# Kernel optimization log

Measured on AMD Instinct MI355X. Metric: run time of the kernel, lower is better.

Reference implementation:

```python
import jax, jax.numpy as jnp
import numpy as np

B, IN, O, F, FH = 512, 2000, 64, 8, 32
D = 64 + FH * O  # 2112


def setup_inputs() -> dict:
    key = jax.random.key(0)
    ks = jax.random.split(key, 17)
    rn = lambda k, s: jax.random.normal(k, s, dtype=jnp.float32) * 0.05
    return dict(
        x=rn(ks[0], (B, IN)),
        fc_in_W=rn(ks[1], (1024, IN)), fc_in_b=rn(ks[2], (1024,)),
        fc1_W=rn(ks[3], (128, 1024)), fc1_b=rn(ks[4], (128,)),
        out1_W=rn(ks[5], (O, 64, 128)), out1_b=rn(ks[6], (O, 64)),
        coef_nn_W=rn(ks[7], (F, FH, 1)), coef_nn_b=rn(ks[8], (F, FH)),
        coef_att_W=rn(ks[9], (F, FH, FH)),
        out_att_W=rn(ks[10], (O, FH, FH)),
        nodes_trans_W=rn(ks[11], (O, O)),
        trans_gcn_W=rn(ks[12], (D, D)),
        outmap_W=rn(ks[13], (1, D)), outmap_b=rn(ks[14], (1,)),
        prelu_a=jnp.float32(0.25),
        coef_m=rn(ks[15], (O, O, F)),
    )


def reference(x, fc_in_W, fc_in_b, fc1_W, fc1_b, out1_W, out1_b,
              coef_nn_W, coef_nn_b, coef_att_W, out_att_W,
              nodes_trans_W, trans_gcn_W, outmap_W, outmap_b, prelu_a, coef_m):
    elu = jax.nn.elu
    # trunk MLP
    h = jax.nn.relu(x @ fc_in_W.T + fc_in_b)          # [B,1024]
    h = jax.nn.relu(h @ fc1_W.T + fc1_b)              # [B,128]
    # per-output-node heads (vectorized over the output_dim loop)
    hiddens = jax.nn.relu(jnp.einsum('bk,odk->bod', h, out1_W) + out1_b)  # [B,O,64]
    # per-feature coef embedding: Linear(1,FH) on each coef_m[:,:,i] slice
    cf = elu(coef_m[..., None] * coef_nn_W[:, :, 0] + coef_nn_b)          # [O,O,F,FH]
    # sum over concatenated feature axis (F*FH) of exp(elu(.))
    s = jnp.exp(elu(cf)).sum(axis=(2, 3))[:, :, None, None]               # [O,O,1,1]
    lin = jnp.einsum('xyfh,fgh->xyfg', cf, coef_att_W)                    # per-feature attention linear
    p = elu(jnp.exp(elu(cf)) * lin / s)
    cfs = elu(p.sum(axis=2) / F)                                          # [O,O,FH]
    # node-level attention (vectorized over the output_dim loop)
    coef_sum = jnp.exp(elu(cfs)).sum(axis=1)                              # [O,FH]
    p2 = jnp.exp(elu(cfs)) / coef_sum[:, None, :]                         # [O,O,FH]
    lin2 = jnp.einsum('oih,igh->oig', cfs, out_att_W)
    att = (p2 * lin2).reshape(O, O * FH)                                  # concat over i (i-major)
    hc = jnp.concatenate(
        [hiddens, jnp.broadcast_to(att[None], (x.shape[0], O, O * FH))], axis=2)  # [B,O,D]
    nt = jnp.einsum('bpd,op->bod', hc, nodes_trans_W)                     # node mixing Linear(O,O)
    trans = jax.nn.sigmoid(jnp.einsum('bod,ed->boe', nt, trans_gcn_W))    # [B,O,D]
    z = (trans @ outmap_W.T + outmap_b).squeeze(-1)                       # [B,O]
    return jnp.where(z >= 0, z, prelu_a * z)                              # PReLU
```

## Files before the change

### kernel.cpp

```cpp
#include <hip/hip_runtime.h>
#include <math.h>

typedef __attribute__((ext_vector_type(8))) short bf16x8;
typedef __attribute__((ext_vector_type(4))) float f32x4;

static __device__ __forceinline__ float fast_elu(float x) {
    return x > 0.0f ? x : __expf(x) - 1.0f;
}

static __device__ __forceinline__ unsigned short f2bf(float f) {
    unsigned int u = __float_as_uint(f);
    unsigned int r = (u + 0x7FFFu + ((u >> 16) & 1u)) >> 16;
    return (unsigned short)r;
}

static __device__ __forceinline__ bf16x8 cvt8(const float* __restrict__ s) {
    float4 a = *reinterpret_cast<const float4*>(s);
    float4 b = *reinterpret_cast<const float4*>(s + 4);
    bf16x8 r;
    r[0] = (short)f2bf(a.x); r[1] = (short)f2bf(a.y);
    r[2] = (short)f2bf(a.z); r[3] = (short)f2bf(a.w);
    r[4] = (short)f2bf(b.x); r[5] = (short)f2bf(b.y);
    r[6] = (short)f2bf(b.z); r[7] = (short)f2bf(b.w);
    return r;
}

#define S0 131072
#define S1 393216
#define S2 409600
#define S3 410112
#define S4 475648
#define S5 492544
#define CONV_BLOCKS 1924

static __device__ __forceinline__ void conv_phase(
    int bx,
    const float* __restrict__ x, const float* __restrict__ fcinW,
    const float* __restrict__ fc1W, const float* __restrict__ ntW,
    const float* __restrict__ out1W, const float* __restrict__ tgw,
    unsigned short* __restrict__ xb, unsigned short* __restrict__ fcinWb,
    unsigned short* __restrict__ fc1Wb, unsigned short* __restrict__ Wb,
    unsigned short* __restrict__ out1WbT, unsigned short* __restrict__ Gb)
{
    int u = bx * 256 + threadIdx.x;
    if (u < S0) {
        int r = u >> 8, c = u & 255;
        bf16x8 v;
        if (c < 250) v = cvt8(&x[(size_t)r * 2000 + c * 8]);
        else { bf16x8 z = {0,0,0,0,0,0,0,0}; v = z; }
        *reinterpret_cast<bf16x8*>(&xb[(size_t)r * 2048 + c * 8]) = v;
    } else if (u < S1) {
        int i = u - S0;
        int r = i >> 8, c = i & 255;
        bf16x8 v;
        if (c < 250) v = cvt8(&fcinW[(size_t)r * 2000 + c * 8]);
        else { bf16x8 z = {0,0,0,0,0,0,0,0}; v = z; }
        *reinterpret_cast<bf16x8*>(&fcinWb[(size_t)r * 2048 + c * 8]) = v;
    } else if (u < S2) {
        int i8 = (u - S1) * 8;
        *reinterpret_cast<bf16x8*>(&fc1Wb[i8]) = cvt8(&fc1W[i8]);
    } else if (u < S3) {
        int i8 = (u - S2) * 8;
        *reinterpret_cast<bf16x8*>(&Wb[i8]) = cvt8(&ntW[i8]);
    } else if (u < S4) {
        int i = u - S3;
        int n = i >> 4, kc = i & 15;
        int d = n >> 6, p = n & 63;
        *reinterpret_cast<bf16x8*>(&out1WbT[(size_t)n * 128 + kc * 8]) =
            cvt8(&out1W[(size_t)((p << 6) | d) * 128 + kc * 8]);
    } else if (u < S5) {
        int i = u - S4;
        int e = i >> 3, c = i & 7;
        *reinterpret_cast<bf16x8*>(&Gb[(size_t)e * 64 + c * 8]) =
            cvt8(&tgw[(size_t)e * 2112 + c * 8]);
    }
}

static __device__ __forceinline__ void coef_phase(
    int bx, float* __restrict__ smemf,
    const float* __restrict__ coef_m, const float* __restrict__ cW,
    const float* __restrict__ cB, const float* __restrict__ attW,
    float* __restrict__ cfs)
{
    float* cf_s = smemf;
    float* part = smemf + 1024;
    const int t = threadIdx.x;
    const int wv = t >> 6, lane = t & 63;
    const int xy = bx * 4 + wv;
    float ls = 0.0f;
    #pragma unroll
    for (int i = 0; i < 4; ++i) {
        int idx = i * 64 + lane;
        int f = idx >> 5;
        float v = fast_elu(coef_m[xy * 8 + f] * cW[idx] + cB[idx]);
        cf_s[wv * 256 + idx] = v;
        ls += __expf(fast_elu(v));
    }
    #pragma unroll
    for (int m = 1; m < 64; m <<= 1) ls += __shfl_xor(ls, m, 64);
    __syncthreads();
    const float rs = __builtin_amdgcn_rcpf(ls);
    const int g = lane & 31, fg = lane >> 5;
    float acc = 0.0f;
    for (int f = fg * 4; f < fg * 4 + 4; ++f) {
        float lin = 0.0f;
        #pragma unroll
        for (int h = 0; h < 32; h += 4) {
            float4 Lv = *reinterpret_cast<const float4*>(&cf_s[wv * 256 + f * 32 + h]);
            float4 Wv = *reinterpret_cast<const float4*>(&attW[f * 1024 + g * 32 + h]);
            lin += Lv.x * Wv.x + Lv.y * Wv.y + Lv.z * Wv.z + Lv.w * Wv.w;
        }
        float e = __expf(fast_elu(cf_s[wv * 256 + f * 32 + g]));
        acc += fast_elu(e * lin * rs);
    }
    part[wv * 64 + lane] = acc;
    __syncthreads();
    if (lane < 32) {
        float tot = part[wv * 64 + lane] + part[wv * 64 + lane + 32];
        cfs[xy * 32 + lane] = fast_elu(tot * 0.125f);
    }
}

static __device__ __forceinline__ void att_phase(
    int o, int ic, float* __restrict__ smemf,
    const float* __restrict__ cfs, const float* __restrict__ oattW,
    float* __restrict__ att)
{
    float* L    = smemf;
    float* red  = smemf + 2048;
    float* csum = smemf + 2304;
    const int t = threadIdx.x;
    #pragma unroll
    for (int j = 0; j < 8; ++j) L[t + 256 * j] = cfs[o * 2048 + t + 256 * j];
    __syncthreads();
    {
        int h = t & 31, ig = t >> 5;
        float ps = 0.0f;
        for (int i = ig * 8; i < ig * 8 + 8; ++i) ps += __expf(fast_elu(L[i * 32 + h]));
        red[t] = ps;
        __syncthreads();
        if (t < 32) {
            float cs = 0.0f;
            #pragma unroll
            for (int j = 0; j < 8; ++j) cs += red[j * 32 + t];
            csum[t] = cs;
        }
        __syncthreads();
    }
    int idx = ic * 256 + t;
    int i = idx >> 5, g = idx & 31;
    float lin2 = 0.0f;
    #pragma unroll
    for (int h = 0; h < 32; h += 4) {
        float4 Lv = *reinterpret_cast<const float4*>(&L[i * 32 + h]);
        float4 Wv = *reinterpret_cast<const float4*>(&oattW[i * 1024 + g * 32 + h]);
        lin2 += Lv.x * Wv.x + Lv.y * Wv.y + Lv.z * Wv.z + Lv.w * Wv.w;
    }
    float p2 = __expf(fast_elu(L[idx])) * __builtin_amdgcn_rcpf(csum[g]);
    att[o * 2048 + idx] = p2 * lin2;
}

static __device__ __forceinline__ void natt_phase(
    int bx, float* __restrict__ smemf,
    const float* __restrict__ ntW, const float* __restrict__ att,
    unsigned short* __restrict__ nattb)
{
    float* ntW_s = smemf;
    float* att_s = smemf + 64 * 65;
    const int t = threadIdx.x;
    const int d0 = bx * 16;
    #pragma unroll
    for (int j = 0; j < 16; ++j) {
        int idx = t + 256 * j;
        ntW_s[(idx >> 6) * 65 + (idx & 63)] = ntW[idx];
    }
    #pragma unroll
    for (int j = 0; j < 4; ++j) {
        int idx = t + 256 * j;
        int p = idx >> 4, dd = idx & 15;
        att_s[p * 17 + dd] = att[p * 2048 + d0 + dd];
    }
    __syncthreads();
    const int dd = t & 15, ob = (t >> 4) * 4;
    float acc[4] = {0.0f, 0.0f, 0.0f, 0.0f};
    for (int p = 0; p < 64; ++p) {
        float av = att_s[p * 17 + dd];
        #pragma unroll
        for (int i = 0; i < 4; ++i) acc[i] += ntW_s[(ob + i) * 65 + p] * av;
    }
    #pragma unroll
    for (int i = 0; i < 4; ++i)
        nattb[(ob + i) * 2048 + d0 + dd] = f2bf(acc[i]);
}

static __device__ __forceinline__ void gemm_core(
    const unsigned short* __restrict__ A, int lda,
    const unsigned short* __restrict__ B, int ldb,
    float* __restrict__ C, unsigned short* __restrict__ Cb,
    int ldc, long strideCz, const float* __restrict__ bias,
    int mode, int kchunk, int bn, int bm, int bz,
    unsigned short* __restrict__ As, unsigned short* __restrict__ Bs)
{
    const int t = threadIdx.x;
    const int w = t >> 6, lane = t & 63, l16 = lane & 15, quad = lane >> 4;
    const int n0 = bn * 64, m0 = bm * 64;
    const int kb0 = bz * kchunk;
    const int r = t >> 2, koff = (t & 3) * 8;
    if (mode == 0) C += (size_t)bz * strideCz;

    const size_t arow = (size_t)(m0 + r) * lda + koff;
    const size_t brow = (size_t)(n0 + r) * ldb + koff;
    bf16x8 av = *reinterpret_cast<const bf16x8*>(&A[arow + kb0]);
    bf16x8 bv = *reinterpret_cast<const bf16x8*>(&B[brow + kb0]);

    f32x4 acc[4] = {};
    for (int kb = kb0; kb < kb0 + kchunk; kb += 32) {
        __syncthreads();
        *reinterpret_cast<bf16x8*>(&As[r * 40 + koff]) = av;
        *reinterpret_cast<bf16x8*>(&Bs[r * 40 + koff]) = bv;
        if (kb + 32 < kb0 + kchunk) {
            av = *reinterpret_cast<const bf16x8*>(&A[arow + kb + 32]);
            bv = *reinterpret_cast<const bf16x8*>(&B[brow + kb + 32]);
        }
        __syncthreads();
        bf16x8 af = *reinterpret_cast<const bf16x8*>(&As[(w * 16 + l16) * 40 + quad * 8]);
        #pragma unroll
        for (int nt = 0; nt < 4; ++nt) {
            bf16x8 bf = *reinterpret_cast<const bf16x8*>(&Bs[(nt * 16 + l16) * 40 + quad * 8]);
            acc[nt] = __builtin_amdgcn_mfma_f32_16x16x32_bf16(af, bf, acc[nt], 0, 0, 0);
        }
    }
    #pragma unroll
    for (int nt = 0; nt < 4; ++nt)
        #pragma unroll
        for (int i = 0; i < 4; ++i) {
            int m = m0 + w * 16 + quad * 4 + i;
            int n = n0 + nt * 16 + l16;
            if (mode == 0) {
                C[(size_t)m * ldc + n] = acc[nt][i];
            } else {
                int bidx = (((n & 63) << 6) | (n >> 6));
                float v = acc[nt][i] + bias[bidx];
                v = fmaxf(v, 0.0f);
                Cb[(size_t)m * ldc + n] = f2bf(v);
            }
        }
}

static __device__ __forceinline__ void gemm_tgwa_core(
    const float* __restrict__ tgw,
    const unsigned short* __restrict__ B,
    float* __restrict__ C, long strideCz,
    int kchunk, int bm, int bz,
    unsigned short* __restrict__ As, unsigned short* __restrict__ Bs)
{
    const int t = threadIdx.x;
    const int w = t >> 6, lane = t & 63, l16 = lane & 15, quad = lane >> 4;
    const int m0 = bm * 64;
    const int kb0 = bz * kchunk;
    const int r = t >> 2, koff = (t & 3) * 8;
    C += (size_t)bz * strideCz;

    const float* arow = tgw + (size_t)(m0 + r) * 2112 + 64 + koff;
    const unsigned short* brow = B + (size_t)r * 2048 + koff;
    bf16x8 av = cvt8(arow + kb0);
    bf16x8 bv = *reinterpret_cast<const bf16x8*>(brow + kb0);

    f32x4 acc[4] = {};
    for (int kb = kb0; kb < kb0 + kchunk; kb += 32) {
        __syncthreads();
        *reinterpret_cast<bf16x8*>(&As[r * 40 + koff]) = av;
        *reinterpret_cast<bf16x8*>(&Bs[r * 40 + koff]) = bv;
        if (kb + 32 < kb0 + kchunk) {
            av = cvt8(arow + kb + 32);
            bv = *reinterpret_cast<const bf16x8*>(brow + kb + 32);
        }
        __syncthreads();
        bf16x8 af = *reinterpret_cast<const bf16x8*>(&As[(w * 16 + l16) * 40 + quad * 8]);
        #pragma unroll
        for (int nt = 0; nt < 4; ++nt) {
            bf16x8 bf = *reinterpret_cast<const bf16x8*>(&Bs[(nt * 16 + l16) * 40 + quad * 8]);
            acc[nt] = __builtin_amdgcn_mfma_f32_16x16x32_bf16(af, bf, acc[nt], 0, 0, 0);
        }
    }
    #pragma unroll
    for (int nt = 0; nt < 4; ++nt)
        #pragma unroll
        for (int i = 0; i < 4; ++i) {
            int m = m0 + w * 16 + quad * 4 + i;
            int n = nt * 16 + l16;
            C[(size_t)m * 64 + n] = acc[nt][i];
        }
}

static __device__ __forceinline__ void gemm_fa_core(
    const float* __restrict__ Ap, int lda, long apstride, int nparts,
    const float* __restrict__ abias,
    const unsigned short* __restrict__ B, int ldb,
    float* __restrict__ C, unsigned short* __restrict__ Cb,
    int ldc, long strideCz, const float* __restrict__ bias,
    int mode, int kchunk, int bn, int bm, int bz,
    unsigned short* __restrict__ As, unsigned short* __restrict__ Bs)
{
    const int t = threadIdx.x;
    const int w = t >> 6, lane = t & 63, l16 = lane & 15, quad = lane >> 4;
    const int n0 = bn * 64, m0 = bm * 64;
    const int kb0 = bz * kchunk;
    const int r = t >> 2, koff = (t & 3) * 8;
    if (mode == 0) C += (size_t)bz * strideCz;

    f32x4 acc[4] = {};
    for (int kb = kb0; kb < kb0 + kchunk; kb += 32) {
        float a8[8];
        {
            const float* base = &Ap[(size_t)(m0 + r) * lda + kb + koff];
            float4 s0 = *reinterpret_cast<const float4*>(base);
            float4 s1 = *reinterpret_cast<const float4*>(base + 4);
            for (int j = 1; j < nparts; ++j) {
                const float* pj = base + (size_t)j * apstride;
                float4 p0 = *reinterpret_cast<const float4*>(pj);
                float4 p1 = *reinterpret_cast<const float4*>(pj + 4);
                s0.x += p0.x; s0.y += p0.y; s0.z += p0.z; s0.w += p0.w;
                s1.x += p1.x; s1.y += p1.y; s1.z += p1.z; s1.w += p1.w;
            }
            float4 b0 = *reinterpret_cast<const float4*>(&abias[kb + koff]);
            float4 b1 = *reinterpret_cast<const float4*>(&abias[kb + koff + 4]);
            a8[0] = fmaxf(s0.x + b0.x, 0.0f); a8[1] = fmaxf(s0.y + b0.y, 0.0f);
            a8[2] = fmaxf(s0.z + b0.z, 0.0f); a8[3] = fmaxf(s0.w + b0.w, 0.0f);
            a8[4] = fmaxf(s1.x + b1.x, 0.0f); a8[5] = fmaxf(s1.y + b1.y, 0.0f);
            a8[6] = fmaxf(s1.z + b1.z, 0.0f); a8[7] = fmaxf(s1.w + b1.w, 0.0f);
        }
        bf16x8 bv = *reinterpret_cast<const bf16x8*>(&B[(size_t)(n0 + r) * ldb + kb + koff]);
        __syncthreads();
        ushort4 lo, hi;
        lo.x = f2bf(a8[0]); lo.y = f2bf(a8[1]); lo.z = f2bf(a8[2]); lo.w = f2bf(a8[3]);
        hi.x = f2bf(a8[4]); hi.y = f2bf(a8[5]); hi.z = f2bf(a8[6]); hi.w = f2bf(a8[7]);
        *reinterpret_cast<ushort4*>(&As[r * 40 + koff]) = lo;
        *reinterpret_cast<ushort4*>(&As[r * 40 + koff + 4]) = hi;
        *reinterpret_cast<bf16x8*>(&Bs[r * 40 + koff]) = bv;
        __syncthreads();
        bf16x8 af = *reinterpret_cast<const bf16x8*>(&As[(w * 16 + l16) * 40 + quad * 8]);
        #pragma unroll
        for (int nt = 0; nt < 4; ++nt) {
            bf16x8 bf = *reinterpret_cast<const bf16x8*>(&Bs[(nt * 16 + l16) * 40 + quad * 8]);
            acc[nt] = __builtin_amdgcn_mfma_f32_16x16x32_bf16(af, bf, acc[nt], 0, 0, 0);
        }
    }
    #pragma unroll
    for (int nt = 0; nt < 4; ++nt)
        #pragma unroll
        for (int i = 0; i < 4; ++i) {
            int m = m0 + w * 16 + quad * 4 + i;
            int n = n0 + nt * 16 + l16;
            if (mode == 0) {
                C[(size_t)m * ldc + n] = acc[nt][i];
            } else {
                int bidx = (((n & 63) << 6) | (n >> 6));
                float v = acc[nt][i] + bias[bidx];
                v = fmaxf(v, 0.0f);
                Cb[(size_t)m * ldc + n] = f2bf(v);
            }
        }
}

static __device__ __forceinline__ void nt1f_phase(
    int b, unsigned short* __restrict__ smemu,
    const unsigned short* __restrict__ hbT, const unsigned short* __restrict__ Wb,
    unsigned short* __restrict__ nt1b)
{
    unsigned short* HtT   = smemu;
    unsigned short* nt1_s = smemu + 64 * 72;
    const int t = threadIdx.x;
    const int w = t >> 6, lane = t & 63, l16 = lane & 15, quad = lane >> 4;

    const unsigned short* src = hbT + (size_t)b * 4096;
    #pragma unroll
    for (int j = 0; j < 2; ++j) {
        int c = t + j * 256;
        *reinterpret_cast<bf16x8*>(&HtT[(c >> 3) * 72 + (c & 7) * 8]) =
            *reinterpret_cast<const bf16x8*>(&src[c * 8]);
    }
    __syncthreads();

    bf16x8 aW[2];
    #pragma unroll
    for (int h = 0; h < 2; ++h)
        aW[h] = *reinterpret_cast<const bf16x8*>(&Wb[(w * 16 + l16) * 64 + h * 32 + quad * 8]);
    #pragma unroll
    for (int dt = 0; dt < 4; ++dt) {
        f32x4 acc = {0.0f, 0.0f, 0.0f, 0.0f};
        #pragma unroll
        for (int h = 0; h < 2; ++h) {
            bf16x8 bf = *reinterpret_cast<const bf16x8*>(
                &HtT[(dt * 16 + l16) * 72 + h * 32 + quad * 8]);
            acc = __builtin_amdgcn_mfma_f32_16x16x32_bf16(aW[h], bf, acc, 0, 0, 0);
        }
        #pragma unroll
        for (int i = 0; i < 4; ++i)
            nt1_s[(w * 16 + quad * 4 + i) * 72 + dt * 16 + l16] = f2bf(acc[i]);
    }
    __syncthreads();
    #pragma unroll
    for (int j = 0; j < 2; ++j) {
        int c = t + j * 256;
        *reinterpret_cast<bf16x8*>(&nt1b[(size_t)b * 4096 + c * 8]) =
            *reinterpret_cast<const bf16x8*>(&nt1_s[(c >> 3) * 72 + (c & 7) * 8]);
    }
}

__global__ __launch_bounds__(256) void uber1(
    const float* x, const float* fcinW, const float* fc1W, const float* ntW,
    const float* out1W, const float* tgw,
    unsigned short* xb, unsigned short* fcinWb, unsigned short* fc1Wb,
    unsigned short* Wb, unsigned short* out1WbT, unsigned short* Gb,
    const float* coef_m, const float* cW, const float* cB, const float* attW,
    float* cfs)
{
    __shared__ __align__(16) float smemf[1280];
    int bx = blockIdx.x;
    if (bx < CONV_BLOCKS)
        conv_phase(bx, x, fcinW, fc1W, ntW, out1W, tgw,
                   xb, fcinWb, fc1Wb, Wb, out1WbT, Gb);
    else
        coef_phase(bx - CONV_BLOCKS, smemf, coef_m, cW, cB, attW, cfs);
}

__global__ __launch_bounds__(256) void uber2(
    const unsigned short* xb, const unsigned short* fcinWb, float* h1p,
    const float* cfs, const float* oattW, float* att)
{
    __shared__ __align__(16) float smemf[2592];
    int bx = blockIdx.x;
    if (bx < 512) {
        unsigned short* As = (unsigned short*)smemf;
        gemm_core(xb, 2048, fcinWb, 2048, h1p, nullptr, 1024, 524288L,
                  nullptr, 0, 512, bx & 15, (bx >> 4) & 7, bx >> 7, As, As + 2560);
    } else {
        int b2 = bx - 512;
        att_phase(b2 & 63, b2 >> 6, smemf, cfs, oattW, att);
    }
}

__global__ __launch_bounds__(256) void uber3(
    const float* h1p, const float* fc_in_b, const unsigned short* fc1Wb,
    float* h2p,
    const float* ntW, const float* att, unsigned short* nattb)
{
    __shared__ __align__(16) float smemf[5248];
    int bx = blockIdx.x;
    if (bx < 64) {
        unsigned short* As = (unsigned short*)smemf;
        gemm_fa_core(h1p, 1024, 524288L, 4, fc_in_b, fc1Wb, 1024,
                     h2p, nullptr, 128, 65536L, nullptr, 0, 256,
                     bx & 1, (bx >> 1) & 7, bx >> 4, As, As + 2560);
    } else {
        natt_phase(bx - 64, smemf, ntW, att, nattb);
    }
}

__global__ __launch_bounds__(256) void uber4(
    const float* h2p, const float* fc1_b, const unsigned short* out1WbT,
    unsigned short* hbT, const float* out1_b,
    const float* tgw, const unsigned short* nattb, float* cpT)
{
    __shared__ __align__(16) float smemf[2560];
    unsigned short* As = (unsigned short*)smemf;
    int bx = blockIdx.x;
    if (bx < 512) {
        gemm_fa_core(h2p, 128, 65536L, 4, fc1_b, out1WbT, 128,
                     nullptr, hbT, 4096, 0L, out1_b, 2, 128,
                     bx & 63, bx >> 6, 0, As, As + 2560);
    } else {
        int b2 = bx - 512;
        gemm_tgwa_core(tgw, nattb, cpT, 135168L, 256,
                       b2 % 33, b2 / 33, As, As + 2560);
    }
}

__global__ __launch_bounds__(256) void uber5(
    const unsigned short* hbT, const unsigned short* Wb, unsigned short* nt1b,
    const float* cpT, float* cmatT)
{
    __shared__ __align__(16) unsigned short smemu[2 * 64 * 72];
    int bx = blockIdx.x;
    if (bx < 512) {
        nt1f_phase(bx, smemu, hbT, Wb, nt1b);
    } else {
        int i = (bx - 512) * 256 + threadIdx.x;
        if (i < 135168) {
            float a = 0.0f;
            #pragma unroll
            for (int j = 0; j < 8; ++j) a += cpT[i + (long)j * 135168L];
            cmatT[i] = a;
        }
    }
}

__global__ __launch_bounds__(256) void final_eblk(
    const unsigned short* __restrict__ nt1b,
    const unsigned short* __restrict__ Gb,
    const float* __restrict__ cmatT,
    const float* __restrict__ outW,
    float* __restrict__ zpart)
{
    __shared__ __align__(16) unsigned short nls[2][64 * 72];
    __shared__ float zs[2][4][64];
    const int t = threadIdx.x;
    const int w = t >> 6, lane = t & 63, l16 = lane & 15, quad = lane >> 4;
    const int eb = blockIdx.x;
    const int b0 = blockIdx.y * 16;
    const int ew = eb * 64 + w * 16;

    bf16x8 ga[2];
    #pragma unroll
    for (int h = 0; h < 2; ++h)
        ga[h] = *reinterpret_cast<const bf16x8*>(
            &Gb[(size_t)(ew + l16) * 64 + h * 32 + quad * 8]);
    float cm[4][4];
    #pragma unroll
    for (int nt = 0; nt < 4; ++nt)
        #pragma unroll
        for (int i = 0; i < 4; ++i)
            cm[nt][i] = cmatT[(size_t)(ew + quad * 4 + i) * 64 + nt * 16 + l16];
    float wv[4];
    #pragma unroll
    for (int i = 0; i < 4; ++i) wv[i] = outW[ew + quad * 4 + i];

    const int c0 = t, c1 = t + 256;
    bf16x8 v0 = *reinterpret_cast<const bf16x8*>(&nt1b[(size_t)b0 * 4096 + c0 * 8]);
    bf16x8 v1 = *reinterpret_cast<const bf16x8*>(&nt1b[(size_t)b0 * 4096 + c1 * 8]);
    *reinterpret_cast<bf16x8*>(&nls[0][(c0 >> 3) * 72 + (c0 & 7) * 8]) = v0;
    *reinterpret_cast<bf16x8*>(&nls[0][(c1 >> 3) * 72 + (c1 & 7) * 8]) = v1;
    __syncthreads();

    int cur = 0;
    for (int bi = 0; bi < 16; ++bi) {
        if (bi < 15) {
            v0 = *reinterpret_cast<const bf16x8*>(
                &nt1b[(size_t)(b0 + bi + 1) * 4096 + c0 * 8]);
            v1 = *reinterpret_cast<const bf16x8*>(
                &nt1b[(size_t)(b0 + bi + 1) * 4096 + c1 * 8]);
        }
        if (bi > 0 && t < 64) {
            const float* z = &zs[(bi - 1) & 1][0][0];
            zpart[((size_t)eb * 512 + b0 + bi - 1) * 64 + t] =
                z[t] + z[64 + t] + z[128 + t] + z[192 + t];
        }
        float zo[4] = {0.0f, 0.0f, 0.0f, 0.0f};
        #pragma unroll
        for (int nt = 0; nt < 4; ++nt) {
            bf16x8 bf0 = *reinterpret_cast<const bf16x8*>(
                &nls[cur][(nt * 16 + l16) * 72 + quad * 8]);
            bf16x8 bf1 = *reinterpret_cast<const bf16x8*>(
                &nls[cur][(nt * 16 + l16) * 72 + 32 + quad * 8]);
            f32x4 acc = {cm[nt][0], cm[nt][1], cm[nt][2], cm[nt][3]};
            acc = __builtin_amdgcn_mfma_f32_16x16x32_bf16(ga[0], bf0, acc, 0, 0, 0);
            acc = __builtin_amdgcn_mfma_f32_16x16x32_bf16(ga[1], bf1, acc, 0, 0, 0);
            #pragma unroll
            for (int i = 0; i < 4; ++i)
                zo[nt] += __builtin_amdgcn_rcpf(1.0f + __expf(-acc[i])) * wv[i];
        }
        #pragma unroll
        for (int nt = 0; nt < 4; ++nt) {
            zo[nt] += __shfl_xor(zo[nt], 16, 64);
            zo[nt] += __shfl_xor(zo[nt], 32, 64);
        }
        if (quad == 0) {
            #pragma unroll
            for (int nt = 0; nt < 4; ++nt)
                zs[bi & 1][w][nt * 16 + l16] = zo[nt];
        }
        if (bi < 15) {
            *reinterpret_cast<bf16x8*>(&nls[1 - cur][(c0 >> 3) * 72 + (c0 & 7) * 8]) = v0;
            *reinterpret_cast<bf16x8*>(&nls[1 - cur][(c1 >> 3) * 72 + (c1 & 7) * 8]) = v1;
        }
        __syncthreads();
        cur ^= 1;
    }
    if (t < 64) {
        const float* z = &zs[1][0][0];
        zpart[((size_t)eb * 512 + b0 + 15) * 64 + t] =
            z[t] + z[64 + t] + z[128 + t] + z[192 + t];
    }
}

__global__ __launch_bounds__(256) void finish_kernel(
    const float* __restrict__ zpart, const float* __restrict__ outB,
    const float* __restrict__ preluA, float* __restrict__ out)
{
    int i = blockIdx.x * 256 + threadIdx.x;
    float z = 0.0f;
    for (int j = 0; j < 33; ++j) z += zpart[(size_t)j * 32768 + i];
    z += outB[0];
    float pa = preluA[0];
    out[i] = (z >= 0.0f) ? z : pa * z;
}

extern "C" void kernel_launch(void* const* d_in, const int* in_sizes, int n_in,
                              void* d_out, int out_size, void* d_ws, size_t ws_size,
                              hipStream_t stream)
{
    const float* x       = (const float*)d_in[0];
    const float* fc_in_W = (const float*)d_in[1];
    const float* fc_in_b = (const float*)d_in[2];
    const float* fc1_W   = (const float*)d_in[3];
    const float* fc1_b   = (const float*)d_in[4];
    const float* out1_W  = (const float*)d_in[5];
    const float* out1_b  = (const float*)d_in[6];
    const float* cW      = (const float*)d_in[7];
    const float* cB      = (const float*)d_in[8];
    const float* cattW   = (const float*)d_in[9];
    const float* oattW   = (const float*)d_in[10];
    const float* ntW     = (const float*)d_in[11];
    const float* tgw     = (const float*)d_in[12];
    const float* outW    = (const float*)d_in[13];
    const float* outB    = (const float*)d_in[14];
    const float* preluA  = (const float*)d_in[15];
    const float* coef_m  = (const float*)d_in[16];
    float* out = (float*)d_out;
    float* ws  = (float*)d_ws;

    unsigned short* xb      = (unsigned short*)(ws + 0);
    unsigned short* fcinWb  = (unsigned short*)(ws + 524288);
    float*          cpT     = ws + 0;
    float*          h1p     = ws + 1572864;
    unsigned short* nt1b    = (unsigned short*)(ws + 1572864);
    float*          zpart   = ws + 2621440;
    unsigned short* fc1Wb   = (unsigned short*)(ws + 3670016);
    float*          h2p     = ws + 3735552;
    unsigned short* out1WbT = (unsigned short*)(ws + 3997696);
    unsigned short* hbT     = (unsigned short*)(ws + 4259840);
    unsigned short* Wb      = (unsigned short*)(ws + 5308416);
    unsigned short* Gb      = (unsigned short*)(ws + 5310464);
    float*          att     = ws + 7540736;
    unsigned short* nattb   = (unsigned short*)(ws + 7671808);
    float*          cmatT   = ws + 7737344;
    float*          cfs     = ws + 7737344;

    uber1<<<CONV_BLOCKS + 1024, 256, 0, stream>>>(
        x, fc_in_W, fc1_W, ntW, out1_W, tgw,
        xb, fcinWb, fc1Wb, Wb, out1WbT, Gb,
        coef_m, cW, cB, cattW, cfs);
    uber2<<<1024, 256, 0, stream>>>(xb, fcinWb, h1p, cfs, oattW, att);
    uber3<<<192, 256, 0, stream>>>(h1p, fc_in_b, fc1Wb, h2p, ntW, att, nattb);
    uber4<<<776, 256, 0, stream>>>(h2p, fc1_b, out1WbT, hbT, out1_b,
                                   tgw, nattb, cpT);
    uber5<<<1040, 256, 0, stream>>>(hbT, Wb, nt1b, cpT, cmatT);
    final_eblk<<<dim3(33, 32), 256, 0, stream>>>(nt1b, Gb, cmatT, outW, zpart);
    finish_kernel<<<128, 256, 0, stream>>>(zpart, outB, preluA, out);
}
```

Before: 194.9 us.

## Fuse nt1, final GEMM, and PReLU into one per-batch kernel; drop split-K

Removes the split-K partition of the tgw·natt GEMM, so 33 blocks each run the full K=2048 and write cmatT directly, which eliminates the separate reduction pass. Merges nt1 computation, the final sigmoid-weighted GEMM over all 33 e-chunks, and the PReLU finish into one per-batch kernel (final2). This drops the nt1b and zpart intermediates and two launches. The trade-off is less parallelism in the tgw GEMM (33 long blocks instead of 264) and 512 blocks that each loop over all of E serially.

```diff
diff --git a/kernel.cpp b/kernel.cpp
--- a/kernel.cpp
+++ b/kernel.cpp
@@ -250,28 +250,26 @@
 static __device__ __forceinline__ void gemm_tgwa_core(
     const float* __restrict__ tgw,
     const unsigned short* __restrict__ B,
-    float* __restrict__ C, long strideCz,
-    int kchunk, int bm, int bz,
+    float* __restrict__ C,
+    int bm,
     unsigned short* __restrict__ As, unsigned short* __restrict__ Bs)
 {
     const int t = threadIdx.x;
     const int w = t >> 6, lane = t & 63, l16 = lane & 15, quad = lane >> 4;
     const int m0 = bm * 64;
-    const int kb0 = bz * kchunk;
     const int r = t >> 2, koff = (t & 3) * 8;
-    C += (size_t)bz * strideCz;
 
     const float* arow = tgw + (size_t)(m0 + r) * 2112 + 64 + koff;
     const unsigned short* brow = B + (size_t)r * 2048 + koff;
-    bf16x8 av = cvt8(arow + kb0);
-    bf16x8 bv = *reinterpret_cast<const bf16x8*>(brow + kb0);
+    bf16x8 av = cvt8(arow);
+    bf16x8 bv = *reinterpret_cast<const bf16x8*>(brow);
 
     f32x4 acc[4] = {};
-    for (int kb = kb0; kb < kb0 + kchunk; kb += 32) {
+    for (int kb = 0; kb < 2048; kb += 32) {
         __syncthreads();
         *reinterpret_cast<bf16x8*>(&As[r * 40 + koff]) = av;
         *reinterpret_cast<bf16x8*>(&Bs[r * 40 + koff]) = bv;
-        if (kb + 32 < kb0 + kchunk) {
+        if (kb + 32 < 2048) {
             av = cvt8(arow + kb + 32);
             bv = *reinterpret_cast<const bf16x8*>(brow + kb + 32);
         }
@@ -363,51 +361,6 @@
         }
 }
 
-static __device__ __forceinline__ void nt1f_phase(
-    int b, unsigned short* __restrict__ smemu,
-    const unsigned short* __restrict__ hbT, const unsigned short* __restrict__ Wb,
-    unsigned short* __restrict__ nt1b)
-{
-    unsigned short* HtT   = smemu;
-    unsigned short* nt1_s = smemu + 64 * 72;
-    const int t = threadIdx.x;
-    const int w = t >> 6, lane = t & 63, l16 = lane & 15, quad = lane >> 4;
-
-    const unsigned short* src = hbT + (size_t)b * 4096;
-    #pragma unroll
-    for (int j = 0; j < 2; ++j) {
-        int c = t + j * 256;
-        *reinterpret_cast<bf16x8*>(&HtT[(c >> 3) * 72 + (c & 7) * 8]) =
-            *reinterpret_cast<const bf16x8*>(&src[c * 8]);
-    }
-    __syncthreads();
-
-    bf16x8 aW[2];
-    #pragma unroll
-    for (int h = 0; h < 2; ++h)
-        aW[h] = *reinterpret_cast<const bf16x8*>(&Wb[(w * 16 + l16) * 64 + h * 32 + quad * 8]);
-    #pragma unroll
-    for (int dt = 0; dt < 4; ++dt) {
-        f32x4 acc = {0.0f, 0.0f, 0.0f, 0.0f};
-        #pragma unroll
-        for (int h = 0; h < 2; ++h) {
-            bf16x8 bf = *reinterpret_cast<const bf16x8*>(
-                &HtT[(dt * 16 + l16) * 72 + h * 32 + quad * 8]);
-            acc = __builtin_amdgcn_mfma_f32_16x16x32_bf16(aW[h], bf, acc, 0, 0, 0);
-        }
-        #pragma unroll
-        for (int i = 0; i < 4; ++i)
-            nt1_s[(w * 16 + quad * 4 + i) * 72 + dt * 16 + l16] = f2bf(acc[i]);
-    }
-    __syncthreads();
-    #pragma unroll
-    for (int j = 0; j < 2; ++j) {
-        int c = t + j * 256;
-        *reinterpret_cast<bf16x8*>(&nt1b[(size_t)b * 4096 + c * 8]) =
-            *reinterpret_cast<const bf16x8*>(&nt1_s[(c >> 3) * 72 + (c & 7) * 8]);
-    }
-}
-
 __global__ __launch_bounds__(256) void uber1(
     const float* x, const float* fcinW, const float* fc1W, const float* ntW,
     const float* out1W, const float* tgw,
@@ -461,7 +414,7 @@
 __global__ __launch_bounds__(256) void uber4(
     const float* h2p, const float* fc1_b, const unsigned short* out1WbT,
     unsigned short* hbT, const float* out1_b,
-    const float* tgw, const unsigned short* nattb, float* cpT)
+    const float* tgw, const unsigned short* nattb, float* cmatT)
 {
     __shared__ __align__(16) float smemf[2560];
     unsigned short* As = (unsigned short*)smemf;
@@ -471,129 +424,125 @@
                      nullptr, hbT, 4096, 0L, out1_b, 2, 128,
                      bx & 63, bx >> 6, 0, As, As + 2560);
     } else {
-        int b2 = bx - 512;
-        gemm_tgwa_core(tgw, nattb, cpT, 135168L, 256,
-                       b2 % 33, b2 / 33, As, As + 2560);
-    }
-}
-
-__global__ __launch_bounds__(256) void uber5(
-    const unsigned short* hbT, const unsigned short* Wb, unsigned short* nt1b,
-    const float* cpT, float* cmatT)
-{
-    __shared__ __align__(16) unsigned short smemu[2 * 64 * 72];
-    int bx = blockIdx.x;
-    if (bx < 512) {
-        nt1f_phase(bx, smemu, hbT, Wb, nt1b);
-    } else {
-        int i = (bx - 512) * 256 + threadIdx.x;
-        if (i < 135168) {
-            float a = 0.0f;
-            #pragma unroll
-            for (int j = 0; j < 8; ++j) a += cpT[i + (long)j * 135168L];
-            cmatT[i] = a;
-        }
-    }
-}
-
-__global__ __launch_bounds__(256) void final_eblk(
-    const unsigned short* __restrict__ nt1b,
+        gemm_tgwa_core(tgw, nattb, cmatT, bx - 512, As, As + 2560);
+    }
+}
+
+__global__ __launch_bounds__(256) void final2(
+    const unsigned short* __restrict__ hbT,
+    const unsigned short* __restrict__ Wb,
     const unsigned short* __restrict__ Gb,
     const float* __restrict__ cmatT,
     const float* __restrict__ outW,
-    float* __restrict__ zpart)
-{
-    __shared__ __align__(16) unsigned short nls[2][64 * 72];
-    __shared__ float zs[2][4][64];
+    const float* __restrict__ outB,
+    const float* __restrict__ preluA,
+    float* __restrict__ out)
+{
+    __shared__ __align__(16) unsigned short HtT[64 * 72];
+    __shared__ __align__(16) unsigned short nt1_s[64 * 72];
+    __shared__ float zp[4][64];
     const int t = threadIdx.x;
     const int w = t >> 6, lane = t & 63, l16 = lane & 15, quad = lane >> 4;
-    const int eb = blockIdx.x;
-    const int b0 = blockIdx.y * 16;
-    const int ew = eb * 64 + w * 16;
-
-    bf16x8 ga[2];
+    const int b = blockIdx.x;
+
+    const unsigned short* src = hbT + (size_t)b * 4096;
+    #pragma unroll
+    for (int j = 0; j < 2; ++j) {
+        int c = t + j * 256;
+        *reinterpret_cast<bf16x8*>(&HtT[(c >> 3) * 72 + (c & 7) * 8]) =
+            *reinterpret_cast<const bf16x8*>(&src[c * 8]);
+    }
+    __syncthreads();
+
+    bf16x8 aW[2];
     #pragma unroll
     for (int h = 0; h < 2; ++h)
-        ga[h] = *reinterpret_cast<const bf16x8*>(
-            &Gb[(size_t)(ew + l16) * 64 + h * 32 + quad * 8]);
-    float cm[4][4];
-    #pragma unroll
-    for (int nt = 0; nt < 4; ++nt)
+        aW[h] = *reinterpret_cast<const bf16x8*>(&Wb[(w * 16 + l16) * 64 + h * 32 + quad * 8]);
+    #pragma unroll
+    for (int dt = 0; dt < 4; ++dt) {
+        f32x4 acc = {0.0f, 0.0f, 0.0f, 0.0f};
+        #pragma unroll
+        for (int h = 0; h < 2; ++h) {
+            bf16x8 bf = *reinterpret_cast<const bf16x8*>(
+                &HtT[(dt * 16 + l16) * 72 + h * 32 + quad * 8]);
+            acc = __builtin_amdgcn_mfma_f32_16x16x32_bf16(aW[h], bf, acc, 0, 0, 0);
+        }
         #pragma unroll
         for (int i = 0; i < 4; ++i)
-            cm[nt][i] = cmatT[(size_t)(ew + quad * 4 + i) * 64 + nt * 16 + l16];
-    float wv[4];
-    #pragma unroll
-    for (int i = 0; i < 4; ++i) wv[i] = outW[ew + quad * 4 + i];
-
-    const int c0 = t, c1 = t + 256;
-    bf16x8 v0 = *reinterpret_cast<const bf16x8*>(&nt1b[(size_t)b0 * 4096 + c0 * 8]);
-    bf16x8 v1 = *reinterpret_cast<const bf16x8*>(&nt1b[(size_t)b0 * 4096 + c1 * 8]);
-    *reinterpret_cast<bf16x8*>(&nls[0][(c0 >> 3) * 72 + (c0 & 7) * 8]) = v0;
-    *reinterpret_cast<bf16x8*>(&nls[0][(c1 >> 3) * 72 + (c1 & 7) * 8]) = v1;
-    __syncthreads();
-
-    int cur = 0;
-    for (int bi = 0; bi < 16; ++bi) {
-        if (bi < 15) {
-            v0 = *reinterpret_cast<const bf16x8*>(
-                &nt1b[(size_t)(b0 + bi + 1) * 4096 + c0 * 8]);
-            v1 = *reinterpret_cast<const bf16x8*>(
-                &nt1b[(size_t)(b0 + bi + 1) * 4096 + c1 * 8]);
-        }
-        if (bi > 0 && t < 64) {
-            const float* z = &zs[(bi - 1) & 1][0][0];
-            zpart[((size_t)eb * 512 + b0 + bi - 1) * 64 + t] =
-                z[t] + z[64 + t] + z[128 + t] + z[192 + t];
-        }
-        float zo[4] = {0.0f, 0.0f, 0.0f, 0.0f};
-        #pragma unroll
-        for (int nt = 0; nt < 4; ++nt) {
-            bf16x8 bf0 = *reinterpret_cast<const bf16x8*>(
-                &nls[cur][(nt * 16 + l16) * 72 + quad * 8]);
-            bf16x8 bf1 = *reinterpret_cast<const bf16x8*>(
-                &nls[cur][(nt * 16 + l16) * 72 + 32 + quad * 8]);
-            f32x4 acc = {cm[nt][0], cm[nt][1], cm[nt][2], cm[nt][3]};
-            acc = __builtin_amdgcn_mfma_f32_16x16x32_bf16(ga[0], bf0, acc, 0, 0, 0);
-            acc = __builtin_amdgcn_mfma_f32_16x16x32_bf16(ga[1], bf1, acc, 0, 0, 0);
+            nt1_s[(w * 16 + quad * 4 + i) * 72 + dt * 16 + l16] = f2bf(acc[i]);
+    }
+    __syncthreads();
+
+    bf16x8 afr[4][2];
+    #pragma unroll
+    for (int ot = 0; ot < 4; ++ot)
+        #pragma unroll
+        for (int h = 0; h < 2; ++h)
+            afr[ot][h] = *reinterpret_cast<const bf16x8*>(
+                &nt1_s[(ot * 16 + l16) * 72 + h * 32 + quad * 8]);
+
+    float zacc[4][4] = {};
+    int e = w * 16 + l16;
+    bf16x8 g0 = *reinterpret_cast<const bf16x8*>(&Gb[(size_t)e * 64 + quad * 8]);
+    bf16x8 g1 = *reinterpret_cast<const bf16x8*>(&Gb[(size_t)e * 64 + 32 + quad * 8]);
+    float wv = outW[e];
+    float4 c4[4];
+    #pragma unroll
+    for (int ot = 0; ot < 4; ++ot)
+        c4[ot] = *reinterpret_cast<const float4*>(&cmatT[(size_t)e * 64 + ot * 16 + quad * 4]);
+
+    for (int ec = 0; ec < 33; ++ec) {
+        const int en = e + 64;
+        const bool more = (ec + 1 < 33);
+        bf16x8 ng0, ng1; float4 nc4[4]; float nwv;
+        if (more) {
+            ng0 = *reinterpret_cast<const bf16x8*>(&Gb[(size_t)en * 64 + quad * 8]);
+            ng1 = *reinterpret_cast<const bf16x8*>(&Gb[(size_t)en * 64 + 32 + quad * 8]);
+            nwv = outW[en];
+            #pragma unroll
+            for (int ot = 0; ot < 4; ++ot)
+                nc4[ot] = *reinterpret_cast<const float4*>(
+                    &cmatT[(size_t)en * 64 + ot * 16 + quad * 4]);
+        }
+        #pragma unroll
+        for (int ot = 0; ot < 4; ++ot) {
+            f32x4 acc = {c4[ot].x, c4[ot].y, c4[ot].z, c4[ot].w};
+            acc = __builtin_amdgcn_mfma_f32_16x16x32_bf16(afr[ot][0], g0, acc, 0, 0, 0);
+            acc = __builtin_amdgcn_mfma_f32_16x16x32_bf16(afr[ot][1], g1, acc, 0, 0, 0);
+            #pragma unroll
+            for (int i = 0; i < 4; ++i) {
+                float sg = __builtin_amdgcn_rcpf(1.0f + __expf(-acc[i]));
+                zacc[ot][i] += sg * wv;
+            }
+        }
+        if (more) {
+            g0 = ng0; g1 = ng1; wv = nwv;
+            #pragma unroll
+            for (int ot = 0; ot < 4; ++ot) c4[ot] = nc4[ot];
+        }
+        e = en;
+    }
+    #pragma unroll
+    for (int m = 1; m < 16; m <<= 1)
+        #pragma unroll
+        for (int ot = 0; ot < 4; ++ot)
             #pragma unroll
             for (int i = 0; i < 4; ++i)
-                zo[nt] += __builtin_amdgcn_rcpf(1.0f + __expf(-acc[i])) * wv[i];
-        }
-        #pragma unroll
-        for (int nt = 0; nt < 4; ++nt) {
-            zo[nt] += __shfl_xor(zo[nt], 16, 64);
-            zo[nt] += __shfl_xor(zo[nt], 32, 64);
-        }
-        if (quad == 0) {
+                zacc[ot][i] += __shfl_xor(zacc[ot][i], m, 64);
+
+    if (l16 == 0) {
+        #pragma unroll
+        for (int ot = 0; ot < 4; ++ot)
             #pragma unroll
-            for (int nt = 0; nt < 4; ++nt)
-                zs[bi & 1][w][nt * 16 + l16] = zo[nt];
-        }
-        if (bi < 15) {
-            *reinterpret_cast<bf16x8*>(&nls[1 - cur][(c0 >> 3) * 72 + (c0 & 7) * 8]) = v0;
-            *reinterpret_cast<bf16x8*>(&nls[1 - cur][(c1 >> 3) * 72 + (c1 & 7) * 8]) = v1;
-        }
-        __syncthreads();
-        cur ^= 1;
-    }
+            for (int i = 0; i < 4; ++i)
+                zp[w][ot * 16 + quad * 4 + i] = zacc[ot][i];
+    }
+    __syncthreads();
     if (t < 64) {
-        const float* z = &zs[1][0][0];
-        zpart[((size_t)eb * 512 + b0 + 15) * 64 + t] =
-            z[t] + z[64 + t] + z[128 + t] + z[192 + t];
-    }
-}
-
-__global__ __launch_bounds__(256) void finish_kernel(
-    const float* __restrict__ zpart, const float* __restrict__ outB,
-    const float* __restrict__ preluA, float* __restrict__ out)
-{
-    int i = blockIdx.x * 256 + threadIdx.x;
-    float z = 0.0f;
-    for (int j = 0; j < 33; ++j) z += zpart[(size_t)j * 32768 + i];
-    z += outB[0];
-    float pa = preluA[0];
-    out[i] = (z >= 0.0f) ? z : pa * z;
+        float z = zp[0][t] + zp[1][t] + zp[2][t] + zp[3][t] + outB[0];
+        float pa = preluA[0];
+        out[b * 64 + t] = (z >= 0.0f) ? z : pa * z;
+    }
 }
 
 extern "C" void kernel_launch(void* const* d_in, const int* in_sizes, int n_in,
@@ -622,10 +571,7 @@
 
     unsigned short* xb      = (unsigned short*)(ws + 0);
     unsigned short* fcinWb  = (unsigned short*)(ws + 524288);
-    float*          cpT     = ws + 0;
     float*          h1p     = ws + 1572864;
-    unsigned short* nt1b    = (unsigned short*)(ws + 1572864);
-    float*          zpart   = ws + 2621440;
     unsigned short* fc1Wb   = (unsigned short*)(ws + 3670016);
     float*          h2p     = ws + 3735552;
     unsigned short* out1WbT = (unsigned short*)(ws + 3997696);
@@ -643,9 +589,7 @@
         coef_m, cW, cB, cattW, cfs);
     uber2<<<1024, 256, 0, stream>>>(xb, fcinWb, h1p, cfs, oattW, att);
     uber3<<<192, 256, 0, stream>>>(h1p, fc_in_b, fc1Wb, h2p, ntW, att, nattb);
-    uber4<<<776, 256, 0, stream>>>(h2p, fc1_b, out1WbT, hbT, out1_b,
-                                   tgw, nattb, cpT);
-    uber5<<<1040, 256, 0, stream>>>(hbT, Wb, nt1b, cpT, cmatT);
-    final_eblk<<<dim3(33, 32), 256, 0, stream>>>(nt1b, Gb, cmatT, outW, zpart);
-    finish_kernel<<<128, 256, 0, stream>>>(zpart, outB, preluA, out);
-}
+    uber4<<<545, 256, 0, stream>>>(h2p, fc1_b, out1WbT, hbT, out1_b,
+                                   tgw, nattb, cmatT);
+    final2<<<512, 256, 0, stream>>>(hbT, Wb, Gb, cmatT, outW, outB, preluA, out);
+}
```

Result: slower. 233.6 us (+19.8%).
